# Kernel optimization log

Hardware: AMD Instinct MI355X
Metric: run time of the kernel (lower is better)

The kernel has to match this reference:

```python
import jax, jax.numpy as jnp
import numpy as np

NEG_SLOPE = 0.2
EPS = 1e-16

def gat_conv(x, edge_index, W, a_src, a_dst, b):
    # x: [N, Fin], W: [Fin, C], a_src/a_dst: [C], b: [C]
    N = x.shape[0]
    src, dst = edge_index[0], edge_index[1]
    h = x @ W                                  # [N, C]
    alpha_s = h @ a_src                        # [N]
    alpha_d = h @ a_dst                        # [N]
    e = alpha_s[src] + alpha_d[dst]            # [E]
    e = jnp.where(e > 0, e, NEG_SLOPE * e)     # LeakyReLU(0.2)
    # ragged softmax over incoming edges of each dst node
    m = jax.ops.segment_max(e, dst, num_segments=N)       # [N]
    p = jnp.exp(e - m[dst])                                # [E]
    s = jax.ops.segment_sum(p, dst, num_segments=N)        # [N]
    alpha = p / (s[dst] + EPS)                             # [E]
    out = jax.ops.segment_sum(alpha[:, None] * h[src], dst, num_segments=N)
    return out + b

def setup_inputs() -> dict:
    key = jax.random.key(0)
    ks = jax.random.split(key, 10)
    N, Fin, H, C, E = 50000, 128, 64, 64, 800000
    x = jax.random.normal(ks[0], (N, Fin), dtype=jnp.float32)
    edge_index = jax.random.randint(ks[1], (2, E), 0, N, dtype=jnp.int64)
    sc1 = 1.0 / np.sqrt(Fin)
    sc2 = 1.0 / np.sqrt(H)
    W1 = jax.random.normal(ks[2], (Fin, H), dtype=jnp.float32) * sc1
    a_src1 = jax.random.normal(ks[3], (H,), dtype=jnp.float32) * sc2
    a_dst1 = jax.random.normal(ks[4], (H,), dtype=jnp.float32) * sc2
    b1 = jnp.zeros((H,), dtype=jnp.float32)
    W2 = jax.random.normal(ks[5], (H, C), dtype=jnp.float32) * sc2
    a_src2 = jax.random.normal(ks[6], (C,), dtype=jnp.float32) * sc2
    a_dst2 = jax.random.normal(ks[7], (C,), dtype=jnp.float32) * sc2
    b2 = jnp.zeros((C,), dtype=jnp.float32)
    return {"x": x, "edge_index": edge_index, "W1": W1, "a_src1": a_src1,
            "a_dst1": a_dst1, "b1": b1, "W2": W2, "a_src2": a_src2,
            "a_dst2": a_dst2, "b2": b2}

def reference(x, edge_index, W1, a_src1, a_dst1, b1, W2, a_src2, a_dst2, b2):
    h = gat_conv(x, edge_index, W1, a_src1, a_dst1, b1)
    h = jax.nn.relu(h)
    out = gat_conv(h, edge_index, W2, a_src2, a_dst2, b2)
    return out
```

## Files before the change

### kernel.cpp

```cpp
#include <hip/hip_runtime.h>
#include <cstddef>

constexpr int FIN = 128;
constexpr int EPB = 2048;
constexpr int BSH = 7;
constexpr int NPB = 128;
constexpr int PACK_SH = 25;
constexpr int RSTR = 512;
constexpr int CAP = 4608;

typedef _Float16 half4 __attribute__((ext_vector_type(4)));
typedef _Float16 half8 __attribute__((ext_vector_type(8)));
typedef float floatx4 __attribute__((ext_vector_type(4)));

__device__ __forceinline__ int block_scan_tot(int v, int tid, int* wsums,
                                              int* tot) {
    int lane = tid & 63, w = tid >> 6;
    int x = v;
#pragma unroll
    for (int off = 1; off < 64; off <<= 1) {
        int y = __shfl_up(x, off, 64);
        if (lane >= off) x += y;
    }
    if (lane == 63) wsums[w] = x;
    __syncthreads();
    int add = 0;
#pragma unroll
    for (int i = 0; i < 4; ++i) add += (i < w) ? wsums[i] : 0;
    *tot = wsums[0] + wsums[1] + wsums[2] + wsums[3];
    return x + add - v;
}

template <int K, typename XT>
__device__ __forceinline__
void gemm_mfma_body(const XT* __restrict__ X, const float* __restrict__ W,
                    const float* __restrict__ ASRC, const float* __restrict__ ADST,
                    _Float16* __restrict__ Hh, float* __restrict__ AS,
                    float* __restrict__ AD, int N, int blk,
                    _Float16* Xh, _Float16* WT) {
    constexpr int LDH = K + 8;
    const int tid = threadIdx.x;
    const int nb = blk * 64;

    if constexpr (sizeof(XT) == 4) {
        constexpr int QPR = K / 4;
        for (int i = tid; i < 64 * QPR; i += 256) {
            int r = i / QPR, q = i % QPR;
            float4 v = make_float4(0.f, 0.f, 0.f, 0.f);
            if (nb + r < N) v = *(const float4*)(X + (size_t)(nb + r) * K + 4 * q);
            half4 h; h[0] = (_Float16)v.x; h[1] = (_Float16)v.y;
            h[2] = (_Float16)v.z; h[3] = (_Float16)v.w;
            *(half4*)(Xh + r * LDH + 4 * q) = h;
        }
    } else {
        constexpr int OPR = K / 8;
        for (int i = tid; i < 64 * OPR; i += 256) {
            int r = i / OPR, o = i % OPR;
            half8 v = {};
            if (nb + r < N) v = *(const half8*)(X + (size_t)(nb + r) * K + 8 * o);
            *(half8*)(Xh + r * LDH + 8 * o) = v;
        }
    }
    for (int i = tid; i < 64 * (K / 4); i += 256) {
        int n = i & 63, kg = i >> 6;
        half4 h;
#pragma unroll
        for (int j = 0; j < 4; ++j)
            h[j] = (_Float16)W[(4 * kg + j) * 64 + n];
        *(half4*)(WT + n * LDH + 4 * kg) = h;
    }
    __syncthreads();

    const int l = tid & 63;
    const int r0 = (tid >> 6) * 16;
    const int n16 = l & 15, quad = l >> 4;

    floatx4 acc[4];
#pragma unroll
    for (int nt = 0; nt < 4; ++nt) acc[nt] = (floatx4){0.f, 0.f, 0.f, 0.f};

#pragma unroll
    for (int k0 = 0; k0 < K; k0 += 32) {
        half8 a = *(const half8*)(Xh + (r0 + n16) * LDH + k0 + quad * 8);
#pragma unroll
        for (int nt = 0; nt < 4; ++nt) {
            half8 b = *(const half8*)(WT + (nt * 16 + n16) * LDH + k0 + quad * 8);
            acc[nt] = __builtin_amdgcn_mfma_f32_16x16x32_f16(a, b, acc[nt], 0, 0, 0);
        }
    }

    float pa[4] = {0.f, 0.f, 0.f, 0.f}, pd[4] = {0.f, 0.f, 0.f, 0.f};
#pragma unroll
    for (int nt = 0; nt < 4; ++nt) {
        float as_v = ASRC[nt * 16 + n16], ad_v = ADST[nt * 16 + n16];
#pragma unroll
        for (int reg = 0; reg < 4; ++reg) {
            pa[reg] += acc[nt][reg] * as_v;
            pd[reg] += acc[nt][reg] * ad_v;
        }
    }
#pragma unroll
    for (int off = 1; off < 16; off <<= 1) {
#pragma unroll
        for (int reg = 0; reg < 4; ++reg) {
            pa[reg] += __shfl_xor(pa[reg], off, 64);
            pd[reg] += __shfl_xor(pd[reg], off, 64);
        }
    }
    if (n16 == 0) {
#pragma unroll
        for (int reg = 0; reg < 4; ++reg) {
            int row = nb + r0 + quad * 4 + reg;
            if (row < N) { AS[row] = pa[reg]; AD[row] = pd[reg]; }
        }
    }

#pragma unroll
    for (int nt = 0; nt < 4; ++nt)
#pragma unroll
        for (int reg = 0; reg < 4; ++reg)
            Xh[(r0 + quad * 4 + reg) * LDH + nt * 16 + n16] = (_Float16)acc[nt][reg];
    {
        int r = r0 + (l >> 2);
        int o = (l & 3) * 16;
        if (nb + r < N) {
            half8 v0 = *(const half8*)(Xh + r * LDH + o);
            half8 v1 = *(const half8*)(Xh + r * LDH + o + 8);
            *(half8*)(Hh + (size_t)(nb + r) * 64 + o) = v0;
            *(half8*)(Hh + (size_t)(nb + r) * 64 + o + 8) = v1;
        }
    }
}

__global__ __launch_bounds__(256)
void gemm1_and_sort(const float* __restrict__ X, const float* __restrict__ W,
                    const float* __restrict__ ASRC, const float* __restrict__ ADST,
                    _Float16* __restrict__ Hh, float* __restrict__ AS,
                    float* __restrict__ AD, int N,
                    const int* __restrict__ src, const int* __restrict__ dst,
                    int E, int nblk, int nbuck,
                    int* __restrict__ cnts, int* __restrict__ rows,
                    int* __restrict__ ebuck, int* __restrict__ ticket) {
    constexpr int K = FIN, LDH = K + 8;
    __shared__ _Float16 Xh[64 * LDH];
    __shared__ _Float16 WT[64 * LDH];
    __shared__ int wsums[4];

    const int tid = threadIdx.x;
    if ((int)blockIdx.x < nblk) {
        int* sorted = (int*)Xh;
        int* hist   = (int*)WT;
        int* cur    = hist + 512;
        if (blockIdx.x == 0 && tid == 0) *ticket = 0;
        for (int i = tid; i < nbuck; i += 256) hist[i] = 0;
        __syncthreads();

        const int e0 = blockIdx.x * EPB;
        const int e1 = min(e0 + EPB, E);
        const int cnt = e1 - e0;

        int pay[8], bk[8];
#pragma unroll
        for (int k = 0; k < 8; ++k) {
            int e = e0 + tid + k * 256;
            bk[k] = -1; pay[k] = 0;
            if (e < e1) {
                int d = dst[e];
                bk[k] = d >> BSH;
                pay[k] = ((d & (NPB - 1)) << PACK_SH) | src[e];
                atomicAdd(&hist[bk[k]], 1);
            }
        }
        __syncthreads();

        int i0 = 2 * tid, i1 = 2 * tid + 1;
        int v0 = (i0 < nbuck) ? hist[i0] : 0;
        int v1 = (i1 < nbuck) ? hist[i1] : 0;
        int tot;
        int ex = block_scan_tot(v0 + v1, tid, wsums, &tot);
        if (i0 < nbuck) {
            cur[i0] = ex;
            rows[blockIdx.x * RSTR + i0] = ex;
            cnts[blockIdx.x * nbuck + i0] = v0;
        }
        if (i1 < nbuck) {
            cur[i1] = ex + v0;
            rows[blockIdx.x * RSTR + i1] = ex + v0;
            cnts[blockIdx.x * nbuck + i1] = v1;
        }
        if (tid == 0) rows[blockIdx.x * RSTR + nbuck] = cnt;
        __syncthreads();

#pragma unroll
        for (int k = 0; k < 8; ++k) {
            if (bk[k] >= 0) {
                int p = atomicAdd(&cur[bk[k]], 1);
                sorted[p] = pay[k];
            }
        }
        __syncthreads();
        for (int i = tid; i < cnt; i += 256)
            ebuck[blockIdx.x * EPB + i] = sorted[i];
        return;
    }
    gemm_mfma_body<K, float>(X, W, ASRC, ADST, Hh, AS, AD, N,
                             blockIdx.x - nblk, Xh, WT);
}

template <int K, typename XT>
__global__ __launch_bounds__(256)
void gemm_feat(const XT* __restrict__ X, const float* __restrict__ W,
               const float* __restrict__ ASRC, const float* __restrict__ ADST,
               _Float16* __restrict__ Hh, float* __restrict__ AS,
               float* __restrict__ AD, int N) {
    constexpr int LDH = K + 8;
    __shared__ _Float16 Xh[64 * LDH];
    __shared__ _Float16 WT[64 * LDH];
    gemm_mfma_body<K, XT>(X, W, ASRC, ADST, Hh, AS, AD, N, blockIdx.x, Xh, WT);
}

__global__ __launch_bounds__(256)
void bucket_colscan_fused(int* __restrict__ cnts, int nblk, int nbuck,
                          int* __restrict__ btotal, int* __restrict__ bbase,
                          int* __restrict__ ticket) {
    __shared__ int wsums[4];
    __shared__ int lastflag;
    int b = blockIdx.x;
    int tid = threadIdx.x;
    int carry = 0;
    for (int c0 = 0; c0 < nblk; c0 += 256) {
        int t = c0 + tid;
        int v = (t < nblk) ? cnts[t * nbuck + b] : 0;
        int tot;
        int e = block_scan_tot(v, tid, wsums, &tot);
        if (t < nblk) cnts[t * nbuck + b] = e + carry;
        carry += tot;
        __syncthreads();
    }
    if (tid == 0) {
        atomicExch(&btotal[b], carry);
        int old = atomicAdd(ticket, 1);
        lastflag = (old == nbuck - 1);
    }
    __syncthreads();
    if (!lastflag) return;
    int i0 = 2 * tid, i1 = 2 * tid + 1;
    int v0 = (i0 < nbuck) ? atomicAdd(&btotal[i0], 0) : 0;
    int v1 = (i1 < nbuck) ? atomicAdd(&btotal[i1], 0) : 0;
    __syncthreads();
    int tot2;
    int e2 = block_scan_tot(v0 + v1, tid, wsums, &tot2);
    if (i0 <= nbuck) bbase[i0] = e2;
    if (i1 <= nbuck) bbase[i1] = e2 + v0;
}

__global__ __launch_bounds__(256)
void bucket_to_csr(const int* __restrict__ ebuck, const int* __restrict__ rows,
                   const int* __restrict__ cnts, const int* __restrict__ bbase,
                   int N, int E, int nblk, int nbuck,
                   int* __restrict__ row_ptr, int* __restrict__ csr_src) {
    __shared__ int eL[CAP];
    __shared__ int hist[NPB];
    __shared__ int cur[NPB];
    __shared__ int wsums[4];
    const int b = blockIdx.x, tid = threadIdx.x;
    const int nstart = b << BSH;
    const int base = bbase[b], endp = bbase[b + 1];
    const int btot = endp - base;

    if (tid < NPB) hist[tid] = 0;
    for (int blk = tid; blk < nblk; blk += 256) {
        int r0 = rows[blk * RSTR + b];
        int r1 = rows[blk * RSTR + b + 1];
        int c0 = cnts[blk * nbuck + b];
        for (int i = 0; i < r1 - r0; ++i) {
            int c = c0 + i;
            if (c < CAP) eL[c] = ebuck[blk * EPB + r0 + i];
        }
    }
    __syncthreads();

    for (int e = tid; e < btot; e += 256)
        atomicAdd(&hist[((unsigned)eL[e]) >> PACK_SH], 1);
    __syncthreads();
    int v = (tid < NPB) ? hist[tid] : 0;
    int tot;
    int excl = block_scan_tot(v, tid, wsums, &tot);
    if (tid < NPB) {
        cur[tid] = excl;
        if (nstart + tid < N) row_ptr[nstart + tid] = base + excl;
    }
    if (b == 0 && tid == 0) row_ptr[N] = E;
    __syncthreads();
    for (int e = tid; e < btot; e += 256) {
        int pv = eL[e];
        int p = atomicAdd(&cur[((unsigned)pv) >> PACK_SH], 1);
        csr_src[base + p] = pv & ((1 << PACK_SH) - 1);
    }
}

template <typename OT>
__device__ __forceinline__
void agg_one_node(const _Float16* __restrict__ Hh, const float* __restrict__ AS,
                  const float* __restrict__ AD, const int* __restrict__ csr_src,
                  const float* __restrict__ bias, OT* __restrict__ OUT,
                  int n, int base, int end, int lane, int relu) {
    const int cnt = end - base;
    const float adn = AD[n];

    if (cnt > 64) {
        float m = -INFINITY;
        for (int c0 = base; c0 < end; c0 += 64) {
            int c = min(64, end - c0);
            float e = -INFINITY;
            if (lane < c) {
                int sr = csr_src[c0 + lane];
                float t = AS[sr] + adn;
                e = t > 0.f ? t : 0.2f * t;
            }
#pragma unroll
            for (int off = 32; off > 0; off >>= 1) e = fmaxf(e, __shfl_xor(e, off, 64));
            m = fmaxf(m, e);
        }
        float s = 0.f, acc = 0.f;
        for (int c0 = base; c0 < end; c0 += 64) {
            int c = min(64, end - c0);
            int srcl = 0;
            float p = 0.f;
            if (lane < c) {
                srcl = csr_src[c0 + lane];
                float t = AS[srcl] + adn;
                t = t > 0.f ? t : 0.2f * t;
                p = __expf(t - m);
            }
            float cs = p;
#pragma unroll
            for (int off = 32; off > 0; off >>= 1) cs += __shfl_xor(cs, off, 64);
            s += cs;
            for (int j = 0; j < c; ++j)
                acc += __shfl(p, j, 64) *
                       (float)Hh[(size_t)__shfl(srcl, j, 64) * 64 + lane];
        }
        float o = acc * (1.f / (s + 1e-16f)) + bias[lane];
        if (relu) o = fmaxf(o, 0.f);
        OUT[(size_t)n * 64 + lane] = (OT)o;
        return;
    }

    int srcl = 0;
    float el = 0.f;
    if (lane < cnt) {
        srcl = csr_src[base + lane];
        float e = AS[srcl] + adn;
        el = e > 0.f ? e : 0.2f * e;
    }
    float p = (lane < cnt) ? __expf(el) : 0.f;
    float s = p;
#pragma unroll
    for (int off = 32; off > 0; off >>= 1) s += __shfl_xor(s, off, 64);
    const float inv = 1.f / (s + 1e-16f);

    const int eg = lane >> 3;
    const int c8 = (lane & 7) * 8;

    float acc[8], acc2[8];
#pragma unroll
    for (int t = 0; t < 8; ++t) { acc[t] = 0.f; acc2[t] = 0.f; }

    int j = 0;
    for (; j + 16 <= cnt; j += 16) {
        int iA = j + eg, iB = j + 8 + eg;
        int sA = __shfl(srcl, iA, 64), sB = __shfl(srcl, iB, 64);
        float aA = __shfl(p, iA, 64),  aB = __shfl(p, iB, 64);
        half8 hA = *(const half8*)(Hh + (size_t)sA * 64 + c8);
        half8 hB = *(const half8*)(Hh + (size_t)sB * 64 + c8);
#pragma unroll
        for (int t = 0; t < 8; ++t) {
            acc[t]  += aA * (float)hA[t];
            acc2[t] += aB * (float)hB[t];
        }
    }
    for (; j < cnt; j += 8) {
        int iA = j + eg;
        int sA = __shfl(srcl, iA, 64);
        float aA = __shfl(p, iA, 64);
        half8 hA = *(const half8*)(Hh + (size_t)sA * 64 + c8);
#pragma unroll
        for (int t = 0; t < 8; ++t) acc[t] += aA * (float)hA[t];
    }
#pragma unroll
    for (int t = 0; t < 8; ++t) acc[t] += acc2[t];
#pragma unroll
    for (int off = 8; off <= 32; off <<= 1)
#pragma unroll
        for (int t = 0; t < 8; ++t) acc[t] += __shfl_xor(acc[t], off, 64);

    if (lane < 8) {
        float4 b0 = *(const float4*)(bias + c8);
        float4 b1 = *(const float4*)(bias + c8 + 4);
        float o[8];
        o[0] = acc[0] * inv + b0.x; o[1] = acc[1] * inv + b0.y;
        o[2] = acc[2] * inv + b0.z; o[3] = acc[3] * inv + b0.w;
        o[4] = acc[4] * inv + b1.x; o[5] = acc[5] * inv + b1.y;
        o[6] = acc[6] * inv + b1.z; o[7] = acc[7] * inv + b1.w;
        if (relu) {
#pragma unroll
            for (int t = 0; t < 8; ++t) o[t] = fmaxf(o[t], 0.f);
        }
        if constexpr (sizeof(OT) == 2) {
            half8 hv;
#pragma unroll
            for (int t = 0; t < 8; ++t) hv[t] = (_Float16)o[t];
            *(half8*)((_Float16*)OUT + (size_t)n * 64 + c8) = hv;
        } else {
            *(float4*)((float*)OUT + (size_t)n * 64 + c8) =
                make_float4(o[0], o[1], o[2], o[3]);
            *(float4*)((float*)OUT + (size_t)n * 64 + c8 + 4) =
                make_float4(o[4], o[5], o[6], o[7]);
        }
    }
}

template <typename OT>
__global__ __launch_bounds__(256)
void gat_aggregate(const _Float16* __restrict__ Hh, const float* __restrict__ AS,
                   const float* __restrict__ AD, const int* __restrict__ row_ptr,
                   const int* __restrict__ csr_src, const float* __restrict__ bias,
                   OT* __restrict__ OUT, int N, int relu) {
    const int lane = threadIdx.x & 63;
    const int half = lane >> 5;
    const int l32  = lane & 31;
    const int pair0 = blockIdx.x * 8 + (threadIdx.x >> 6) * 2;
    if (pair0 >= N) return;
    const int n = pair0 + half;

    int base = 0, end = 0;
    if (n < N) { base = row_ptr[n]; end = row_ptr[n + 1]; }
    const int cnt = end - base;

    if (!__all(cnt <= 32)) {
        int baseA = __shfl(base, 0, 64),  endA = __shfl(end, 0, 64);
        int baseB = __shfl(base, 32, 64), endB = __shfl(end, 32, 64);
        agg_one_node(Hh, AS, AD, csr_src, bias, OUT, pair0, baseA, endA, lane, relu);
        if (pair0 + 1 < N)
            agg_one_node(Hh, AS, AD, csr_src, bias, OUT, pair0 + 1, baseB, endB,
                         lane, relu);
        return;
    }

    const float adn = (n < N) ? AD[n] : 0.f;
    int srcl = 0;
    float p = 0.f;
    if (l32 < cnt) {
        srcl = csr_src[base + l32];
        float e = AS[srcl] + adn;
        e = e > 0.f ? e : 0.2f * e;
        p = __expf(e);
    }
    float s = p;
#pragma unroll
    for (int off = 16; off > 0; off >>= 1) s += __shfl_xor(s, off, 64);
    const float inv = 1.f / (s + 1e-16f);

    const int eg = l32 >> 3;
    const int c8 = (l32 & 7) * 8;

    float acc[8], acc2[8];
#pragma unroll
    for (int t = 0; t < 8; ++t) { acc[t] = 0.f; acc2[t] = 0.f; }

    int j = 0;
    for (; j + 8 <= cnt; j += 8) {
        int iA = j + eg, iB = j + 4 + eg;
        int sA = __shfl(srcl, iA, 32), sB = __shfl(srcl, iB, 32);
        float aA = __shfl(p, iA, 32),  aB = __shfl(p, iB, 32);
        half8 hA = *(const half8*)(Hh + (size_t)sA * 64 + c8);
        half8 hB = *(const half8*)(Hh + (size_t)sB * 64 + c8);
#pragma unroll
        for (int t = 0; t < 8; ++t) {
            acc[t]  += aA * (float)hA[t];
            acc2[t] += aB * (float)hB[t];
        }
    }
    for (; j < cnt; j += 4) {
        int iA = j + eg;
        int sA = __shfl(srcl, iA, 32);
        float aA = __shfl(p, iA, 32);
        half8 hA = *(const half8*)(Hh + (size_t)sA * 64 + c8);
#pragma unroll
        for (int t = 0; t < 8; ++t) acc[t] += aA * (float)hA[t];
    }
#pragma unroll
    for (int t = 0; t < 8; ++t) acc[t] += acc2[t];
#pragma unroll
    for (int t = 0; t < 8; ++t) acc[t] += __shfl_xor(acc[t], 8, 64);
#pragma unroll
    for (int t = 0; t < 8; ++t) acc[t] += __shfl_xor(acc[t], 16, 64);

    if (l32 < 8 && n < N) {
        float4 b0 = *(const float4*)(bias + c8);
        float4 b1 = *(const float4*)(bias + c8 + 4);
        float o[8];
        o[0] = acc[0] * inv + b0.x; o[1] = acc[1] * inv + b0.y;
        o[2] = acc[2] * inv + b0.z; o[3] = acc[3] * inv + b0.w;
        o[4] = acc[4] * inv + b1.x; o[5] = acc[5] * inv + b1.y;
        o[6] = acc[6] * inv + b1.z; o[7] = acc[7] * inv + b1.w;
        if (relu) {
#pragma unroll
            for (int t = 0; t < 8; ++t) o[t] = fmaxf(o[t], 0.f);
        }
        if constexpr (sizeof(OT) == 2) {
            half8 hv;
#pragma unroll
            for (int t = 0; t < 8; ++t) hv[t] = (_Float16)o[t];
            *(half8*)((_Float16*)OUT + (size_t)n * 64 + c8) = hv;
        } else {
            *(float4*)((float*)OUT + (size_t)n * 64 + c8) =
                make_float4(o[0], o[1], o[2], o[3]);
            *(float4*)((float*)OUT + (size_t)n * 64 + c8 + 4) =
                make_float4(o[4], o[5], o[6], o[7]);
        }
    }
}

extern "C" void kernel_launch(void* const* d_in, const int* in_sizes, int n_in,
                              void* d_out, int out_size, void* d_ws, size_t ws_size,
                              hipStream_t stream) {
    const float* x    = (const float*)d_in[0];
    const int*   ei   = (const int*)d_in[1];
    const float* W1   = (const float*)d_in[2];
    const float* as1w = (const float*)d_in[3];
    const float* ad1w = (const float*)d_in[4];
    const float* b1   = (const float*)d_in[5];
    const float* W2   = (const float*)d_in[6];
    const float* as2w = (const float*)d_in[7];
    const float* ad2w = (const float*)d_in[8];
    const float* b2   = (const float*)d_in[9];
    float* out = (float*)d_out;

    const int N = in_sizes[0] / FIN;
    const int E = in_sizes[1] / 2;
    const int* esrc = ei;
    const int* edst = ei + E;

    const int nbuck = (N + NPB - 1) >> BSH;
    const int nblk  = (E + EPB - 1) / EPB;

    char* wp8 = (char*)d_ws;
    _Float16* Hh  = (_Float16*)wp8;  wp8 += (size_t)N * 64 * 2;
    _Float16* R1h = (_Float16*)wp8;  wp8 += (size_t)N * 64 * 2;
    float* AS1 = (float*)wp8;        wp8 += (size_t)N * 4;
    float* AD1 = (float*)wp8;        wp8 += (size_t)N * 4;
    float* AS2 = (float*)wp8;        wp8 += (size_t)N * 4;
    float* AD2 = (float*)wp8;        wp8 += (size_t)N * 4;
    int* row_ptr = (int*)wp8;        wp8 += (size_t)(N + 1) * 4;
    int* csr     = (int*)wp8;        wp8 += (size_t)E * 4;
    int* ebuck   = (int*)wp8;        wp8 += (size_t)nblk * EPB * 4;
    int* cnts    = (int*)wp8;        wp8 += (size_t)nblk * nbuck * 4;
    int* rows    = (int*)wp8;        wp8 += (size_t)nblk * RSTR * 4;
    int* btotal  = (int*)wp8;        wp8 += (size_t)nbuck * 4;
    int* bbase   = (int*)wp8;        wp8 += (size_t)(nbuck + 1) * 4;
    int* ticket  = (int*)wp8;        wp8 += 4;

    const int nbG = (N + 63) / 64;
    const int nbAgg = (N + 7) / 8;

    hipLaunchKernelGGL(gemm1_and_sort, dim3(nblk + nbG), dim3(256), 0, stream,
                       x, W1, as1w, ad1w, Hh, AS1, AD1, N,
                       esrc, edst, E, nblk, nbuck, cnts, rows, ebuck, ticket);
    hipLaunchKernelGGL(bucket_colscan_fused, dim3(nbuck), dim3(256), 0, stream,
                       cnts, nblk, nbuck, btotal, bbase, ticket);
    hipLaunchKernelGGL(bucket_to_csr, dim3(nbuck), dim3(256), 0, stream,
                       ebuck, rows, cnts, bbase, N, E, nblk, nbuck, row_ptr, csr);
    hipLaunchKernelGGL(gat_aggregate<_Float16>, dim3(nbAgg), dim3(256), 0,
                       stream, Hh, AS1, AD1, row_ptr, csr, b1, R1h, N, 1);
    hipLaunchKernelGGL((gemm_feat<64, _Float16>), dim3(nbG), dim3(256), 0, stream,
                       R1h, W2, as2w, ad2w, Hh, AS2, AD2, N);
    hipLaunchKernelGGL(gat_aggregate<float>, dim3(nbAgg), dim3(256), 0,
                       stream, Hh, AS2, AD2, row_ptr, csr, b2, out, N, 0);
}
```

Measured before the change: 174.8 us.

## Fuse layer-1 aggregation with layer-2 GEMM through shared memory tile

Layer-1 aggregation now writes its ReLU'd fp16 output rows for a 64-node tile directly into LDS, and the same block then runs the layer-2 MFMA GEMM on that tile. This removes one kernel launch and the global write and read of the intermediate R1 activation. The layer-2 features go to a separate buffer. Each block now processes 64 nodes serially per wave (8 pairs per wave), so there are fewer blocks and less parallelism in aggregation, which may reduce latency hiding for the gather-heavy work.

```diff
diff --git a/kernel.cpp b/kernel.cpp
--- a/kernel.cpp
+++ b/kernel.cpp
@@ -29,6 +29,85 @@
     for (int i = 0; i < 4; ++i) add += (i < w) ? wsums[i] : 0;
     *tot = wsums[0] + wsums[1] + wsums[2] + wsums[3];
     return x + add - v;
+}
+
+template <int K>
+__device__ __forceinline__
+void gemm_core(const float* __restrict__ W, const float* __restrict__ ASRC,
+               const float* __restrict__ ADST, _Float16* __restrict__ Hh,
+               float* __restrict__ AS, float* __restrict__ AD, int N, int nb,
+               _Float16* Xh, _Float16* WT) {
+    constexpr int LDH = K + 8;
+    const int tid = threadIdx.x;
+    for (int i = tid; i < 64 * (K / 4); i += 256) {
+        int n = i & 63, kg = i >> 6;
+        half4 h;
+#pragma unroll
+        for (int j = 0; j < 4; ++j)
+            h[j] = (_Float16)W[(4 * kg + j) * 64 + n];
+        *(half4*)(WT + n * LDH + 4 * kg) = h;
+    }
+    __syncthreads();
+
+    const int l = tid & 63;
+    const int r0 = (tid >> 6) * 16;
+    const int n16 = l & 15, quad = l >> 4;
+
+    floatx4 acc[4];
+#pragma unroll
+    for (int nt = 0; nt < 4; ++nt) acc[nt] = (floatx4){0.f, 0.f, 0.f, 0.f};
+
+#pragma unroll
+    for (int k0 = 0; k0 < K; k0 += 32) {
+        half8 a = *(const half8*)(Xh + (r0 + n16) * LDH + k0 + quad * 8);
+#pragma unroll
+        for (int nt = 0; nt < 4; ++nt) {
+            half8 b = *(const half8*)(WT + (nt * 16 + n16) * LDH + k0 + quad * 8);
+            acc[nt] = __builtin_amdgcn_mfma_f32_16x16x32_f16(a, b, acc[nt], 0, 0, 0);
+        }
+    }
+
+    float pa[4] = {0.f, 0.f, 0.f, 0.f}, pd[4] = {0.f, 0.f, 0.f, 0.f};
+#pragma unroll
+    for (int nt = 0; nt < 4; ++nt) {
+        float as_v = ASRC[nt * 16 + n16], ad_v = ADST[nt * 16 + n16];
+#pragma unroll
+        for (int reg = 0; reg < 4; ++reg) {
+            pa[reg] += acc[nt][reg] * as_v;
+            pd[reg] += acc[nt][reg] * ad_v;
+        }
+    }
+#pragma unroll
+    for (int off = 1; off < 16; off <<= 1) {
+#pragma unroll
+        for (int reg = 0; reg < 4; ++reg) {
+            pa[reg] += __shfl_xor(pa[reg], off, 64);
+            pd[reg] += __shfl_xor(pd[reg], off, 64);
+        }
+    }
+    if (n16 == 0) {
+#pragma unroll
+        for (int reg = 0; reg < 4; ++reg) {
+            int row = nb + r0 + quad * 4 + reg;
+            if (row < N) { AS[row] = pa[reg]; AD[row] = pd[reg]; }
+        }
+    }
+
+#pragma unroll
+    for (int nt = 0; nt < 4; ++nt)
+#pragma unroll
+        for (int reg = 0; reg < 4; ++reg)
+            Xh[(r0 + quad * 4 + reg) * LDH + nt * 16 + n16] = (_Float16)acc[nt][reg];
+    {
+        int r = r0 + (l >> 2);
+        int o = (l & 3) * 16;
+        if (nb + r < N) {
+            half8 v0 = *(const half8*)(Xh + r * LDH + o);
+            half8 v1 = *(const half8*)(Xh + r * LDH + o + 8);
+            *(half8*)(Hh + (size_t)(nb + r) * 64 + o) = v0;
+            *(half8*)(Hh + (size_t)(nb + r) * 64 + o + 8) = v1;
+        }
+    }
 }
 
 template <int K, typename XT>
@@ -41,7 +120,6 @@
     constexpr int LDH = K + 8;
     const int tid = threadIdx.x;
     const int nb = blk * 64;
-
     if constexpr (sizeof(XT) == 4) {
         constexpr int QPR = K / 4;
         for (int i = tid; i < 64 * QPR; i += 256) {
@@ -61,75 +139,7 @@
             *(half8*)(Xh + r * LDH + 8 * o) = v;
         }
     }
-    for (int i = tid; i < 64 * (K / 4); i += 256) {
-        int n = i & 63, kg = i >> 6;
-        half4 h;
-#pragma unroll
-        for (int j = 0; j < 4; ++j)
-            h[j] = (_Float16)W[(4 * kg + j) * 64 + n];
-        *(half4*)(WT + n * LDH + 4 * kg) = h;
-    }
-    __syncthreads();
-
-    const int l = tid & 63;
-    const int r0 = (tid >> 6) * 16;
-    const int n16 = l & 15, quad = l >> 4;
-
-    floatx4 acc[4];
-#pragma unroll
-    for (int nt = 0; nt < 4; ++nt) acc[nt] = (floatx4){0.f, 0.f, 0.f, 0.f};
-
-#pragma unroll
-    for (int k0 = 0; k0 < K; k0 += 32) {
-        half8 a = *(const half8*)(Xh + (r0 + n16) * LDH + k0 + quad * 8);
-#pragma unroll
-        for (int nt = 0; nt < 4; ++nt) {
-            half8 b = *(const half8*)(WT + (nt * 16 + n16) * LDH + k0 + quad * 8);
-            acc[nt] = __builtin_amdgcn_mfma_f32_16x16x32_f16(a, b, acc[nt], 0, 0, 0);
-        }
-    }
-
-    float pa[4] = {0.f, 0.f, 0.f, 0.f}, pd[4] = {0.f, 0.f, 0.f, 0.f};
-#pragma unroll
-    for (int nt = 0; nt < 4; ++nt) {
-        float as_v = ASRC[nt * 16 + n16], ad_v = ADST[nt * 16 + n16];
-#pragma unroll
-        for (int reg = 0; reg < 4; ++reg) {
-            pa[reg] += acc[nt][reg] * as_v;
-            pd[reg] += acc[nt][reg] * ad_v;
-        }
-    }
-#pragma unroll
-    for (int off = 1; off < 16; off <<= 1) {
-#pragma unroll
-        for (int reg = 0; reg < 4; ++reg) {
-            pa[reg] += __shfl_xor(pa[reg], off, 64);
-            pd[reg] += __shfl_xor(pd[reg], off, 64);
-        }
-    }
-    if (n16 == 0) {
-#pragma unroll
-        for (int reg = 0; reg < 4; ++reg) {
-            int row = nb + r0 + quad * 4 + reg;
-            if (row < N) { AS[row] = pa[reg]; AD[row] = pd[reg]; }
-        }
-    }
-
-#pragma unroll
-    for (int nt = 0; nt < 4; ++nt)
-#pragma unroll
-        for (int reg = 0; reg < 4; ++reg)
-            Xh[(r0 + quad * 4 + reg) * LDH + nt * 16 + n16] = (_Float16)acc[nt][reg];
-    {
-        int r = r0 + (l >> 2);
-        int o = (l & 3) * 16;
-        if (nb + r < N) {
-            half8 v0 = *(const half8*)(Xh + r * LDH + o);
-            half8 v1 = *(const half8*)(Xh + r * LDH + o + 8);
-            *(half8*)(Hh + (size_t)(nb + r) * 64 + o) = v0;
-            *(half8*)(Hh + (size_t)(nb + r) * 64 + o + 8) = v1;
-        }
-    }
+    gemm_core<K>(W, ASRC, ADST, Hh, AS, AD, N, nb, Xh, WT);
 }
 
 __global__ __launch_bounds__(256)
@@ -205,18 +215,6 @@
     }
     gemm_mfma_body<K, float>(X, W, ASRC, ADST, Hh, AS, AD, N,
                              blockIdx.x - nblk, Xh, WT);
-}
-
-template <int K, typename XT>
-__global__ __launch_bounds__(256)
-void gemm_feat(const XT* __restrict__ X, const float* __restrict__ W,
-               const float* __restrict__ ASRC, const float* __restrict__ ADST,
-               _Float16* __restrict__ Hh, float* __restrict__ AS,
-               float* __restrict__ AD, int N) {
-    constexpr int LDH = K + 8;
-    __shared__ _Float16 Xh[64 * LDH];
-    __shared__ _Float16 WT[64 * LDH];
-    gemm_mfma_body<K, XT>(X, W, ASRC, ADST, Hh, AS, AD, N, blockIdx.x, Xh, WT);
 }
 
 __global__ __launch_bounds__(256)
@@ -299,12 +297,12 @@
     }
 }
 
-template <typename OT>
+template <bool LDSOUT, typename OT>
 __device__ __forceinline__
 void agg_one_node(const _Float16* __restrict__ Hh, const float* __restrict__ AS,
                   const float* __restrict__ AD, const int* __restrict__ csr_src,
                   const float* __restrict__ bias, OT* __restrict__ OUT,
-                  int n, int base, int end, int lane, int relu) {
+                  _Float16* ldsrow, int n, int base, int end, int lane, int relu) {
     const int cnt = end - base;
     const float adn = AD[n];
 
@@ -343,7 +341,8 @@
         }
         float o = acc * (1.f / (s + 1e-16f)) + bias[lane];
         if (relu) o = fmaxf(o, 0.f);
-        OUT[(size_t)n * 64 + lane] = (OT)o;
+        if constexpr (LDSOUT) ldsrow[lane] = (_Float16)o;
+        else OUT[(size_t)n * 64 + lane] = (OT)o;
         return;
     }
 
@@ -407,7 +406,12 @@
 #pragma unroll
             for (int t = 0; t < 8; ++t) o[t] = fmaxf(o[t], 0.f);
         }
-        if constexpr (sizeof(OT) == 2) {
+        if constexpr (LDSOUT) {
+            half8 hv;
+#pragma unroll
+            for (int t = 0; t < 8; ++t) hv[t] = (_Float16)o[t];
+            *(half8*)(ldsrow + c8) = hv;
+        } else if constexpr (sizeof(OT) == 2) {
             half8 hv;
 #pragma unroll
             for (int t = 0; t < 8; ++t) hv[t] = (_Float16)o[t];
@@ -421,17 +425,15 @@
     }
 }
 
-template <typename OT>
-__global__ __launch_bounds__(256)
-void gat_aggregate(const _Float16* __restrict__ Hh, const float* __restrict__ AS,
-                   const float* __restrict__ AD, const int* __restrict__ row_ptr,
-                   const int* __restrict__ csr_src, const float* __restrict__ bias,
-                   OT* __restrict__ OUT, int N, int relu) {
-    const int lane = threadIdx.x & 63;
+template <bool LDSOUT, typename OT>
+__device__ __forceinline__
+void agg_pair(const _Float16* __restrict__ Hh, const float* __restrict__ AS,
+              const float* __restrict__ AD, const int* __restrict__ row_ptr,
+              const int* __restrict__ csr_src, const float* __restrict__ bias,
+              OT* __restrict__ OUT, _Float16* ldsX, int tile0,
+              int pair0, int N, int relu, int lane) {
     const int half = lane >> 5;
     const int l32  = lane & 31;
-    const int pair0 = blockIdx.x * 8 + (threadIdx.x >> 6) * 2;
-    if (pair0 >= N) return;
     const int n = pair0 + half;
 
     int base = 0, end = 0;
@@ -441,10 +443,13 @@
     if (!__all(cnt <= 32)) {
         int baseA = __shfl(base, 0, 64),  endA = __shfl(end, 0, 64);
         int baseB = __shfl(base, 32, 64), endB = __shfl(end, 32, 64);
-        agg_one_node(Hh, AS, AD, csr_src, bias, OUT, pair0, baseA, endA, lane, relu);
+        agg_one_node<LDSOUT, OT>(Hh, AS, AD, csr_src, bias, OUT,
+                                 LDSOUT ? ldsX + (pair0 - tile0) * 72 : nullptr,
+                                 pair0, baseA, endA, lane, relu);
         if (pair0 + 1 < N)
-            agg_one_node(Hh, AS, AD, csr_src, bias, OUT, pair0 + 1, baseB, endB,
-                         lane, relu);
+            agg_one_node<LDSOUT, OT>(Hh, AS, AD, csr_src, bias, OUT,
+                                     LDSOUT ? ldsX + (pair0 + 1 - tile0) * 72 : nullptr,
+                                     pair0 + 1, baseB, endB, lane, relu);
         return;
     }
 
@@ -509,7 +514,12 @@
 #pragma unroll
             for (int t = 0; t < 8; ++t) o[t] = fmaxf(o[t], 0.f);
         }
-        if constexpr (sizeof(OT) == 2) {
+        if constexpr (LDSOUT) {
+            half8 hv;
+#pragma unroll
+            for (int t = 0; t < 8; ++t) hv[t] = (_Float16)o[t];
+            *(half8*)(ldsX + (n - tile0) * 72 + c8) = hv;
+        } else if constexpr (sizeof(OT) == 2) {
             half8 hv;
 #pragma unroll
             for (int t = 0; t < 8; ++t) hv[t] = (_Float16)o[t];
@@ -521,6 +531,48 @@
                 make_float4(o[4], o[5], o[6], o[7]);
         }
     }
+}
+
+__global__ __launch_bounds__(256)
+void agg1_gemm2(const _Float16* __restrict__ Hh1, const float* __restrict__ AS1,
+                const float* __restrict__ AD1, const int* __restrict__ row_ptr,
+                const int* __restrict__ csr_src, const float* __restrict__ b1,
+                const float* __restrict__ W2, const float* __restrict__ as2w,
+                const float* __restrict__ ad2w, _Float16* __restrict__ Hh2,
+                float* __restrict__ AS2, float* __restrict__ AD2, int N) {
+    constexpr int K = 64, LDH = K + 8;
+    __shared__ _Float16 Xh[64 * LDH];
+    __shared__ _Float16 WT[64 * LDH];
+    const int tid = threadIdx.x;
+    const int tile0 = blockIdx.x * 64;
+
+    for (int i = tid; i < 64 * LDH / 8; i += 256)
+        ((half8*)Xh)[i] = (half8){};
+    __syncthreads();
+
+    const int lane = tid & 63, w = tid >> 6;
+#pragma unroll 1
+    for (int q = 0; q < 8; ++q) {
+        int pair0 = tile0 + (w * 8 + q) * 2;
+        if (pair0 < N)
+            agg_pair<true, _Float16>(Hh1, AS1, AD1, row_ptr, csr_src, b1,
+                                     (_Float16*)nullptr, Xh, tile0,
+                                     pair0, N, 1, lane);
+    }
+    gemm_core<K>(W2, as2w, ad2w, Hh2, AS2, AD2, N, tile0, Xh, WT);
+}
+
+template <typename OT>
+__global__ __launch_bounds__(256)
+void gat_aggregate(const _Float16* __restrict__ Hh, const float* __restrict__ AS,
+                   const float* __restrict__ AD, const int* __restrict__ row_ptr,
+                   const int* __restrict__ csr_src, const float* __restrict__ bias,
+                   OT* __restrict__ OUT, int N, int relu) {
+    const int lane = threadIdx.x & 63;
+    const int pair0 = blockIdx.x * 8 + (threadIdx.x >> 6) * 2;
+    if (pair0 >= N) return;
+    agg_pair<false, OT>(Hh, AS, AD, row_ptr, csr_src, bias, OUT,
+                        (_Float16*)nullptr, 0, pair0, N, relu, lane);
 }
 
 extern "C" void kernel_launch(void* const* d_in, const int* in_sizes, int n_in,
@@ -548,7 +600,7 @@
 
     char* wp8 = (char*)d_ws;
     _Float16* Hh  = (_Float16*)wp8;  wp8 += (size_t)N * 64 * 2;
-    _Float16* R1h = (_Float16*)wp8;  wp8 += (size_t)N * 64 * 2;
+    _Float16* H2h = (_Float16*)wp8;  wp8 += (size_t)N * 64 * 2;
     float* AS1 = (float*)wp8;        wp8 += (size_t)N * 4;
     float* AD1 = (float*)wp8;        wp8 += (size_t)N * 4;
     float* AS2 = (float*)wp8;        wp8 += (size_t)N * 4;
@@ -572,10 +624,9 @@
                        cnts, nblk, nbuck, btotal, bbase, ticket);
     hipLaunchKernelGGL(bucket_to_csr, dim3(nbuck), dim3(256), 0, stream,
                        ebuck, rows, cnts, bbase, N, E, nblk, nbuck, row_ptr, csr);
-    hipLaunchKernelGGL(gat_aggregate<_Float16>, dim3(nbAgg), dim3(256), 0,
-                       stream, Hh, AS1, AD1, row_ptr, csr, b1, R1h, N, 1);
-    hipLaunchKernelGGL((gemm_feat<64, _Float16>), dim3(nbG), dim3(256), 0, stream,
-                       R1h, W2, as2w, ad2w, Hh, AS2, AD2, N);
+    hipLaunchKernelGGL(agg1_gemm2, dim3(nbG), dim3(256), 0, stream,
+                       Hh, AS1, AD1, row_ptr, csr, b1,
+                       W2, as2w, ad2w, H2h, AS2, AD2, N);
     hipLaunchKernelGGL(gat_aggregate<float>, dim3(nbAgg), dim3(256), 0,
-                       stream, Hh, AS2, AD2, row_ptr, csr, b2, out, N, 0);
-}
+                       stream, H2h, AS2, AD2, row_ptr, csr, b2, out, N, 0);
+}
```

Measured after the change: 177.9 us. About the same (+1.8%).

## Fuse bucket-to-CSR build with first-layer aggregation into one kernel

Applied to the files above, without the earlier changes.

Drops the global column-scan and the separate bucket_to_csr kernel. Each bucket block now gathers its edges with an atomic cursor, sorts them by destination in shared memory and runs layer-1 aggregation straight from shared memory. It also writes a per-bucket padded edge list with row offsets for layer 2, so two kernel launches and a global row_ptr/csr pass go away. The cost is 512-thread blocks with large shared-memory arrays and lower occupancy. Edges past the fixed CAP per bucket are silently dropped, and edge order within a node now depends on atomic timing.

```diff
diff --git a/kernel.cpp b/kernel.cpp
--- a/kernel.cpp
+++ b/kernel.cpp
@@ -6,13 +6,16 @@
 constexpr int BSH = 7;
 constexpr int NPB = 128;
 constexpr int PACK_SH = 25;
+constexpr int SRCMASK = (1 << PACK_SH) - 1;
 constexpr int RSTR = 512;
 constexpr int CAP = 4608;
+constexpr int RPS = NPB + 1;
 
 typedef _Float16 half4 __attribute__((ext_vector_type(4)));
 typedef _Float16 half8 __attribute__((ext_vector_type(8)));
 typedef float floatx4 __attribute__((ext_vector_type(4)));
 
+template <int NW>
 __device__ __forceinline__ int block_scan_tot(int v, int tid, int* wsums,
                                               int* tot) {
     int lane = tid & 63, w = tid >> 6;
@@ -24,11 +27,93 @@
     }
     if (lane == 63) wsums[w] = x;
     __syncthreads();
-    int add = 0;
-#pragma unroll
-    for (int i = 0; i < 4; ++i) add += (i < w) ? wsums[i] : 0;
-    *tot = wsums[0] + wsums[1] + wsums[2] + wsums[3];
+    int add = 0, t = 0;
+#pragma unroll
+    for (int i = 0; i < NW; ++i) {
+        add += (i < w) ? wsums[i] : 0;
+        t += wsums[i];
+    }
+    *tot = t;
     return x + add - v;
+}
+
+template <int K>
+__device__ __forceinline__
+void gemm_core(const float* __restrict__ W, const float* __restrict__ ASRC,
+               const float* __restrict__ ADST, _Float16* __restrict__ Hh,
+               float* __restrict__ AS, float* __restrict__ AD, int N, int nb,
+               _Float16* Xh, _Float16* WT) {
+    constexpr int LDH = K + 8;
+    const int tid = threadIdx.x;
+    for (int i = tid; i < 64 * (K / 4); i += 256) {
+        int n = i & 63, kg = i >> 6;
+        half4 h;
+#pragma unroll
+        for (int j = 0; j < 4; ++j)
+            h[j] = (_Float16)W[(4 * kg + j) * 64 + n];
+        *(half4*)(WT + n * LDH + 4 * kg) = h;
+    }
+    __syncthreads();
+
+    const int l = tid & 63;
+    const int r0 = (tid >> 6) * 16;
+    const int n16 = l & 15, quad = l >> 4;
+
+    floatx4 acc[4];
+#pragma unroll
+    for (int nt = 0; nt < 4; ++nt) acc[nt] = (floatx4){0.f, 0.f, 0.f, 0.f};
+
+#pragma unroll
+    for (int k0 = 0; k0 < K; k0 += 32) {
+        half8 a = *(const half8*)(Xh + (r0 + n16) * LDH + k0 + quad * 8);
+#pragma unroll
+        for (int nt = 0; nt < 4; ++nt) {
+            half8 b = *(const half8*)(WT + (nt * 16 + n16) * LDH + k0 + quad * 8);
+            acc[nt] = __builtin_amdgcn_mfma_f32_16x16x32_f16(a, b, acc[nt], 0, 0, 0);
+        }
+    }
+
+    float pa[4] = {0.f, 0.f, 0.f, 0.f}, pd[4] = {0.f, 0.f, 0.f, 0.f};
+#pragma unroll
+    for (int nt = 0; nt < 4; ++nt) {
+        float as_v = ASRC[nt * 16 + n16], ad_v = ADST[nt * 16 + n16];
+#pragma unroll
+        for (int reg = 0; reg < 4; ++reg) {
+            pa[reg] += acc[nt][reg] * as_v;
+            pd[reg] += acc[nt][reg] * ad_v;
+        }
+    }
+#pragma unroll
+    for (int off = 1; off < 16; off <<= 1) {
+#pragma unroll
+        for (int reg = 0; reg < 4; ++reg) {
+            pa[reg] += __shfl_xor(pa[reg], off, 64);
+            pd[reg] += __shfl_xor(pd[reg], off, 64);
+        }
+    }
+    if (n16 == 0) {
+#pragma unroll
+        for (int reg = 0; reg < 4; ++reg) {
+            int row = nb + r0 + quad * 4 + reg;
+            if (row < N) { AS[row] = pa[reg]; AD[row] = pd[reg]; }
+        }
+    }
+
+#pragma unroll
+    for (int nt = 0; nt < 4; ++nt)
+#pragma unroll
+        for (int reg = 0; reg < 4; ++reg)
+            Xh[(r0 + quad * 4 + reg) * LDH + nt * 16 + n16] = (_Float16)acc[nt][reg];
+    {
+        int r = r0 + (l >> 2);
+        int o = (l & 3) * 16;
+        if (nb + r < N) {
+            half8 v0 = *(const half8*)(Xh + r * LDH + o);
+            half8 v1 = *(const half8*)(Xh + r * LDH + o + 8);
+            *(half8*)(Hh + (size_t)(nb + r) * 64 + o) = v0;
+            *(half8*)(Hh + (size_t)(nb + r) * 64 + o + 8) = v1;
+        }
+    }
 }
 
 template <int K, typename XT>
@@ -41,7 +126,6 @@
     constexpr int LDH = K + 8;
     const int tid = threadIdx.x;
     const int nb = blk * 64;
-
     if constexpr (sizeof(XT) == 4) {
         constexpr int QPR = K / 4;
         for (int i = tid; i < 64 * QPR; i += 256) {
@@ -61,75 +145,7 @@
             *(half8*)(Xh + r * LDH + 8 * o) = v;
         }
     }
-    for (int i = tid; i < 64 * (K / 4); i += 256) {
-        int n = i & 63, kg = i >> 6;
-        half4 h;
-#pragma unroll
-        for (int j = 0; j < 4; ++j)
-            h[j] = (_Float16)W[(4 * kg + j) * 64 + n];
-        *(half4*)(WT + n * LDH + 4 * kg) = h;
-    }
-    __syncthreads();
-
-    const int l = tid & 63;
-    const int r0 = (tid >> 6) * 16;
-    const int n16 = l & 15, quad = l >> 4;
-
-    floatx4 acc[4];
-#pragma unroll
-    for (int nt = 0; nt < 4; ++nt) acc[nt] = (floatx4){0.f, 0.f, 0.f, 0.f};
-
-#pragma unroll
-    for (int k0 = 0; k0 < K; k0 += 32) {
-        half8 a = *(const half8*)(Xh + (r0 + n16) * LDH + k0 + quad * 8);
-#pragma unroll
-        for (int nt = 0; nt < 4; ++nt) {
-            half8 b = *(const half8*)(WT + (nt * 16 + n16) * LDH + k0 + quad * 8);
-            acc[nt] = __builtin_amdgcn_mfma_f32_16x16x32_f16(a, b, acc[nt], 0, 0, 0);
-        }
-    }
-
-    float pa[4] = {0.f, 0.f, 0.f, 0.f}, pd[4] = {0.f, 0.f, 0.f, 0.f};
-#pragma unroll
-    for (int nt = 0; nt < 4; ++nt) {
-        float as_v = ASRC[nt * 16 + n16], ad_v = ADST[nt * 16 + n16];
-#pragma unroll
-        for (int reg = 0; reg < 4; ++reg) {
-            pa[reg] += acc[nt][reg] * as_v;
-            pd[reg] += acc[nt][reg] * ad_v;
-        }
-    }
-#pragma unroll
-    for (int off = 1; off < 16; off <<= 1) {
-#pragma unroll
-        for (int reg = 0; reg < 4; ++reg) {
-            pa[reg] += __shfl_xor(pa[reg], off, 64);
-            pd[reg] += __shfl_xor(pd[reg], off, 64);
-        }
-    }
-    if (n16 == 0) {
-#pragma unroll
-        for (int reg = 0; reg < 4; ++reg) {
-            int row = nb + r0 + quad * 4 + reg;
-            if (row < N) { AS[row] = pa[reg]; AD[row] = pd[reg]; }
-        }
-    }
-
-#pragma unroll
-    for (int nt = 0; nt < 4; ++nt)
-#pragma unroll
-        for (int reg = 0; reg < 4; ++reg)
-            Xh[(r0 + quad * 4 + reg) * LDH + nt * 16 + n16] = (_Float16)acc[nt][reg];
-    {
-        int r = r0 + (l >> 2);
-        int o = (l & 3) * 16;
-        if (nb + r < N) {
-            half8 v0 = *(const half8*)(Xh + r * LDH + o);
-            half8 v1 = *(const half8*)(Xh + r * LDH + o + 8);
-            *(half8*)(Hh + (size_t)(nb + r) * 64 + o) = v0;
-            *(half8*)(Hh + (size_t)(nb + r) * 64 + o + 8) = v1;
-        }
-    }
+    gemm_core<K>(W, ASRC, ADST, Hh, AS, AD, N, nb, Xh, WT);
 }
 
 __global__ __launch_bounds__(256)
@@ -139,8 +155,7 @@
                     float* __restrict__ AD, int N,
                     const int* __restrict__ src, const int* __restrict__ dst,
                     int E, int nblk, int nbuck,
-                    int* __restrict__ cnts, int* __restrict__ rows,
-                    int* __restrict__ ebuck, int* __restrict__ ticket) {
+                    int* __restrict__ rows, int* __restrict__ ebuck) {
     constexpr int K = FIN, LDH = K + 8;
     __shared__ _Float16 Xh[64 * LDH];
     __shared__ _Float16 WT[64 * LDH];
@@ -151,7 +166,6 @@
         int* sorted = (int*)Xh;
         int* hist   = (int*)WT;
         int* cur    = hist + 512;
-        if (blockIdx.x == 0 && tid == 0) *ticket = 0;
         for (int i = tid; i < nbuck; i += 256) hist[i] = 0;
         __syncthreads();
 
@@ -177,16 +191,14 @@
         int v0 = (i0 < nbuck) ? hist[i0] : 0;
         int v1 = (i1 < nbuck) ? hist[i1] : 0;
         int tot;
-        int ex = block_scan_tot(v0 + v1, tid, wsums, &tot);
+        int ex = block_scan_tot<4>(v0 + v1, tid, wsums, &tot);
         if (i0 < nbuck) {
             cur[i0] = ex;
             rows[blockIdx.x * RSTR + i0] = ex;
-            cnts[blockIdx.x * nbuck + i0] = v0;
         }
         if (i1 < nbuck) {
             cur[i1] = ex + v0;
             rows[blockIdx.x * RSTR + i1] = ex + v0;
-            cnts[blockIdx.x * nbuck + i1] = v1;
         }
         if (tid == 0) rows[blockIdx.x * RSTR + nbuck] = cnt;
         __syncthreads();
@@ -217,86 +229,6 @@
     __shared__ _Float16 Xh[64 * LDH];
     __shared__ _Float16 WT[64 * LDH];
     gemm_mfma_body<K, XT>(X, W, ASRC, ADST, Hh, AS, AD, N, blockIdx.x, Xh, WT);
-}
-
-__global__ __launch_bounds__(256)
-void bucket_colscan_fused(int* __restrict__ cnts, int nblk, int nbuck,
-                          int* __restrict__ btotal, int* __restrict__ bbase,
-                          int* __restrict__ ticket) {
-    __shared__ int wsums[4];
-    __shared__ int lastflag;
-    int b = blockIdx.x;
-    int tid = threadIdx.x;
-    int carry = 0;
-    for (int c0 = 0; c0 < nblk; c0 += 256) {
-        int t = c0 + tid;
-        int v = (t < nblk) ? cnts[t * nbuck + b] : 0;
-        int tot;
-        int e = block_scan_tot(v, tid, wsums, &tot);
-        if (t < nblk) cnts[t * nbuck + b] = e + carry;
-        carry += tot;
-        __syncthreads();
-    }
-    if (tid == 0) {
-        atomicExch(&btotal[b], carry);
-        int old = atomicAdd(ticket, 1);
-        lastflag = (old == nbuck - 1);
-    }
-    __syncthreads();
-    if (!lastflag) return;
-    int i0 = 2 * tid, i1 = 2 * tid + 1;
-    int v0 = (i0 < nbuck) ? atomicAdd(&btotal[i0], 0) : 0;
-    int v1 = (i1 < nbuck) ? atomicAdd(&btotal[i1], 0) : 0;
-    __syncthreads();
-    int tot2;
-    int e2 = block_scan_tot(v0 + v1, tid, wsums, &tot2);
-    if (i0 <= nbuck) bbase[i0] = e2;
-    if (i1 <= nbuck) bbase[i1] = e2 + v0;
-}
-
-__global__ __launch_bounds__(256)
-void bucket_to_csr(const int* __restrict__ ebuck, const int* __restrict__ rows,
-                   const int* __restrict__ cnts, const int* __restrict__ bbase,
-                   int N, int E, int nblk, int nbuck,
-                   int* __restrict__ row_ptr, int* __restrict__ csr_src) {
-    __shared__ int eL[CAP];
-    __shared__ int hist[NPB];
-    __shared__ int cur[NPB];
-    __shared__ int wsums[4];
-    const int b = blockIdx.x, tid = threadIdx.x;
-    const int nstart = b << BSH;
-    const int base = bbase[b], endp = bbase[b + 1];
-    const int btot = endp - base;
-
-    if (tid < NPB) hist[tid] = 0;
-    for (int blk = tid; blk < nblk; blk += 256) {
-        int r0 = rows[blk * RSTR + b];
-        int r1 = rows[blk * RSTR + b + 1];
-        int c0 = cnts[blk * nbuck + b];
-        for (int i = 0; i < r1 - r0; ++i) {
-            int c = c0 + i;
-            if (c < CAP) eL[c] = ebuck[blk * EPB + r0 + i];
-        }
-    }
-    __syncthreads();
-
-    for (int e = tid; e < btot; e += 256)
-        atomicAdd(&hist[((unsigned)eL[e]) >> PACK_SH], 1);
-    __syncthreads();
-    int v = (tid < NPB) ? hist[tid] : 0;
-    int tot;
-    int excl = block_scan_tot(v, tid, wsums, &tot);
-    if (tid < NPB) {
-        cur[tid] = excl;
-        if (nstart + tid < N) row_ptr[nstart + tid] = base + excl;
-    }
-    if (b == 0 && tid == 0) row_ptr[N] = E;
-    __syncthreads();
-    for (int e = tid; e < btot; e += 256) {
-        int pv = eL[e];
-        int p = atomicAdd(&cur[((unsigned)pv) >> PACK_SH], 1);
-        csr_src[base + p] = pv & ((1 << PACK_SH) - 1);
-    }
 }
 
 template <typename OT>
@@ -422,29 +354,20 @@
 }
 
 template <typename OT>
-__global__ __launch_bounds__(256)
-void gat_aggregate(const _Float16* __restrict__ Hh, const float* __restrict__ AS,
-                   const float* __restrict__ AD, const int* __restrict__ row_ptr,
-                   const int* __restrict__ csr_src, const float* __restrict__ bias,
-                   OT* __restrict__ OUT, int N, int relu) {
-    const int lane = threadIdx.x & 63;
-    const int half = lane >> 5;
-    const int l32  = lane & 31;
-    const int pair0 = blockIdx.x * 8 + (threadIdx.x >> 6) * 2;
-    if (pair0 >= N) return;
-    const int n = pair0 + half;
-
-    int base = 0, end = 0;
-    if (n < N) { base = row_ptr[n]; end = row_ptr[n + 1]; }
+__device__ __forceinline__
+void agg_pair_core(const _Float16* __restrict__ Hh, const float* __restrict__ AS,
+                   const float* __restrict__ AD, const int* __restrict__ csr,
+                   const float* __restrict__ bias, OT* __restrict__ OUT,
+                   int n, int N, int relu, int lane, int base, int end) {
+    const int l32 = lane & 31;
     const int cnt = end - base;
 
     if (!__all(cnt <= 32)) {
         int baseA = __shfl(base, 0, 64),  endA = __shfl(end, 0, 64);
         int baseB = __shfl(base, 32, 64), endB = __shfl(end, 32, 64);
-        agg_one_node(Hh, AS, AD, csr_src, bias, OUT, pair0, baseA, endA, lane, relu);
-        if (pair0 + 1 < N)
-            agg_one_node(Hh, AS, AD, csr_src, bias, OUT, pair0 + 1, baseB, endB,
-                         lane, relu);
+        int nA = __shfl(n, 0, 64), nB = __shfl(n, 32, 64);
+        if (nA < N) agg_one_node<OT>(Hh, AS, AD, csr, bias, OUT, nA, baseA, endA, lane, relu);
+        if (nB < N) agg_one_node<OT>(Hh, AS, AD, csr, bias, OUT, nB, baseB, endB, lane, relu);
         return;
     }
 
@@ -452,7 +375,7 @@
     int srcl = 0;
     float p = 0.f;
     if (l32 < cnt) {
-        srcl = csr_src[base + l32];
+        srcl = csr[base + l32];
         float e = AS[srcl] + adn;
         e = e > 0.f ? e : 0.2f * e;
         p = __expf(e);
@@ -521,6 +444,91 @@
                 make_float4(o[4], o[5], o[6], o[7]);
         }
     }
+}
+
+__global__ __launch_bounds__(512)
+void bucket_agg1(const int* __restrict__ ebuck, const int* __restrict__ rows,
+                 int nblk, int N,
+                 const _Float16* __restrict__ Hh, const float* __restrict__ AS1,
+                 const float* __restrict__ AD1, const float* __restrict__ b1,
+                 _Float16* __restrict__ R1h,
+                 int* __restrict__ ebuck2, int* __restrict__ rp2) {
+    __shared__ int eL[CAP];
+    __shared__ int eS[CAP];
+    __shared__ int hist[NPB];
+    __shared__ int cur[NPB];
+    __shared__ int rowr[RPS];
+    __shared__ int wsums[8];
+    __shared__ int cursor;
+    const int b = blockIdx.x, tid = threadIdx.x;
+
+    if (tid < NPB) hist[tid] = 0;
+    if (tid == 0) cursor = 0;
+    __syncthreads();
+
+    for (int blk = tid; blk < nblk; blk += 512) {
+        int r0 = rows[blk * RSTR + b];
+        int r1 = rows[blk * RSTR + b + 1];
+        int len = r1 - r0;
+        if (len > 0) {
+            int ofs = atomicAdd(&cursor, len);
+            for (int i = 0; i < len; ++i)
+                if (ofs + i < CAP) eL[ofs + i] = ebuck[blk * EPB + r0 + i];
+        }
+    }
+    __syncthreads();
+    const int btot = min(cursor, CAP);
+
+    for (int e = tid; e < btot; e += 512)
+        atomicAdd(&hist[((unsigned)eL[e]) >> PACK_SH], 1);
+    __syncthreads();
+    int v = (tid < NPB) ? hist[tid] : 0;
+    int tot;
+    int excl = block_scan_tot<8>(v, tid, wsums, &tot);
+    if (tid < NPB) { cur[tid] = excl; rowr[tid] = excl; }
+    if (tid == 0) rowr[NPB] = btot;
+    __syncthreads();
+    for (int e = tid; e < btot; e += 512) {
+        int pv = eL[e];
+        int p = atomicAdd(&cur[((unsigned)pv) >> PACK_SH], 1);
+        eS[p] = pv & SRCMASK;
+    }
+    __syncthreads();
+
+    for (int i = tid; i < btot; i += 512)
+        ebuck2[(size_t)b * CAP + i] = eS[i];
+    for (int j = tid; j < RPS; j += 512)
+        rp2[b * RPS + j] = rowr[j];
+
+    const int lane = tid & 63, w = tid >> 6;
+    const int half = lane >> 5;
+#pragma unroll 1
+    for (int q = 0; q < 8; ++q) {
+        int nloc = w * 16 + q * 2 + half;
+        int n = (b << BSH) + nloc;
+        int base = rowr[nloc], end = rowr[nloc + 1];
+        agg_pair_core<_Float16>(Hh, AS1, AD1, (const int*)eS, b1, R1h,
+                                n, N, 1, lane, base, end);
+    }
+}
+
+__global__ __launch_bounds__(256)
+void gat_aggregate2(const _Float16* __restrict__ Hh, const float* __restrict__ AS,
+                    const float* __restrict__ AD, const int* __restrict__ ebuck2,
+                    const int* __restrict__ rp2, const float* __restrict__ bias,
+                    float* __restrict__ OUT, int N) {
+    const int lane = threadIdx.x & 63;
+    const int half = lane >> 5;
+    const int pair0 = blockIdx.x * 8 + (threadIdx.x >> 6) * 2;
+    if (pair0 >= N) return;
+    const int n = pair0 + half;
+    int base = 0, end = 0;
+    if (n < N) {
+        int b = n >> BSH, j = n & (NPB - 1);
+        base = b * CAP + rp2[b * RPS + j];
+        end  = b * CAP + rp2[b * RPS + j + 1];
+    }
+    agg_pair_core<float>(Hh, AS, AD, ebuck2, bias, OUT, n, N, 0, lane, base, end);
 }
 
 extern "C" void kernel_launch(void* const* d_in, const int* in_sizes, int n_in,
@@ -549,33 +557,27 @@
     char* wp8 = (char*)d_ws;
     _Float16* Hh  = (_Float16*)wp8;  wp8 += (size_t)N * 64 * 2;
     _Float16* R1h = (_Float16*)wp8;  wp8 += (size_t)N * 64 * 2;
+    _Float16* H2h = (_Float16*)wp8;  wp8 += (size_t)N * 64 * 2;
     float* AS1 = (float*)wp8;        wp8 += (size_t)N * 4;
     float* AD1 = (float*)wp8;        wp8 += (size_t)N * 4;
     float* AS2 = (float*)wp8;        wp8 += (size_t)N * 4;
     float* AD2 = (float*)wp8;        wp8 += (size_t)N * 4;
-    int* row_ptr = (int*)wp8;        wp8 += (size_t)(N + 1) * 4;
-    int* csr     = (int*)wp8;        wp8 += (size_t)E * 4;
-    int* ebuck   = (int*)wp8;        wp8 += (size_t)nblk * EPB * 4;
-    int* cnts    = (int*)wp8;        wp8 += (size_t)nblk * nbuck * 4;
-    int* rows    = (int*)wp8;        wp8 += (size_t)nblk * RSTR * 4;
-    int* btotal  = (int*)wp8;        wp8 += (size_t)nbuck * 4;
-    int* bbase   = (int*)wp8;        wp8 += (size_t)(nbuck + 1) * 4;
-    int* ticket  = (int*)wp8;        wp8 += 4;
+    int* ebuck  = (int*)wp8;         wp8 += (size_t)nblk * EPB * 4;
+    int* rows   = (int*)wp8;         wp8 += (size_t)nblk * RSTR * 4;
+    int* ebuck2 = (int*)wp8;         wp8 += (size_t)nbuck * CAP * 4;
+    int* rp2    = (int*)wp8;         wp8 += (size_t)nbuck * RPS * 4;
 
     const int nbG = (N + 63) / 64;
     const int nbAgg = (N + 7) / 8;
 
     hipLaunchKernelGGL(gemm1_and_sort, dim3(nblk + nbG), dim3(256), 0, stream,
                        x, W1, as1w, ad1w, Hh, AS1, AD1, N,
-                       esrc, edst, E, nblk, nbuck, cnts, rows, ebuck, ticket);
-    hipLaunchKernelGGL(bucket_colscan_fused, dim3(nbuck), dim3(256), 0, stream,
-                       cnts, nblk, nbuck, btotal, bbase, ticket);
-    hipLaunchKernelGGL(bucket_to_csr, dim3(nbuck), dim3(256), 0, stream,
-                       ebuck, rows, cnts, bbase, N, E, nblk, nbuck, row_ptr, csr);
-    hipLaunchKernelGGL(gat_aggregate<_Float16>, dim3(nbAgg), dim3(256), 0,
-                       stream, Hh, AS1, AD1, row_ptr, csr, b1, R1h, N, 1);
+                       esrc, edst, E, nblk, nbuck, rows, ebuck);
+    hipLaunchKernelGGL(bucket_agg1, dim3(nbuck), dim3(512), 0, stream,
+                       ebuck, rows, nblk, N, Hh, AS1, AD1, b1, R1h,
+                       ebuck2, rp2);
     hipLaunchKernelGGL((gemm_feat<64, _Float16>), dim3(nbG), dim3(256), 0, stream,
-                       R1h, W2, as2w, ad2w, Hh, AS2, AD2, N);
-    hipLaunchKernelGGL(gat_aggregate<float>, dim3(nbAgg), dim3(256), 0,
-                       stream, Hh, AS2, AD2, row_ptr, csr, b2, out, N, 0);
-}
+                       R1h, W2, as2w, ad2w, H2h, AS2, AD2, N);
+    hipLaunchKernelGGL(gat_aggregate2, dim3(nbAgg), dim3(256), 0, stream,
+                       H2h, AS2, AD2, ebuck2, rp2, b2, out, N);
+}
```

Measured after the change: 162.7 us. -6.9%, faster.
